# Performance work log

Measured on AMD Instinct MI355X. Metric: run time of the kernel, lower is better.

## Reference

```python
import jax, jax.numpy as jnp
import numpy as np

H, D, EPS = 4, 16, 1e-5
N_NODES, N_EDGES, F_IN, HID, N_GRAPHS, N_CLASSES = 100000, 1600000, 128, 64, 512, 10


def _bn(x, g, b, m, v):
    # BatchNorm1d in eval mode: running stats
    return (x - m) * jax.lax.rsqrt(v + EPS) * g + b


def _tconv(x, src, dst, wq, bq, wk, bk, wv, bv, ws, bs):
    # PyG TransformerConv: q from dst node, k/v from src node, scatter-softmax over dst,
    # scatter-add aggregation, concat heads, plus root (skip) linear. Dropout=eval (identity).
    N = x.shape[0]
    q = (x @ wq + bq).reshape(N, H, D)
    k = (x @ wk + bk).reshape(N, H, D)
    v = (x @ wv + bv).reshape(N, H, D)
    alpha = (q[dst] * k[src]).sum(-1) * np.float32(1.0 / np.sqrt(D))  # [E, H]
    amax = jax.ops.segment_max(alpha, dst, num_segments=N)            # [N, H]
    amax = jnp.where(jnp.isfinite(amax), amax, 0.0)
    ex = jnp.exp(alpha - amax[dst])
    denom = jax.ops.segment_sum(ex, dst, num_segments=N)
    attn = ex / (denom[dst] + 1e-16)                                  # [E, H]
    agg = jax.ops.segment_sum(attn[:, :, None] * v[src], dst, num_segments=N)  # [N, H, D]
    return agg.reshape(N, H * D) + x @ ws + bs


def setup_inputs() -> dict:
    key = jax.random.key(0)
    ks = list(jax.random.split(key, 40))
    def w(i, shape):
        return jax.random.normal(ks[i], shape, jnp.float32) * 0.05
    inp = {}
    inp['x'] = jax.random.normal(ks[0], (N_NODES, F_IN), jnp.float32)
    inp['edge_index'] = jax.random.randint(ks[1], (2, N_EDGES), 0, N_NODES, dtype=jnp.int32)
    inp['batch'] = jnp.sort(jax.random.randint(ks[2], (N_NODES,), 0, N_GRAPHS, dtype=jnp.int32))
    i = 3
    for p, fin in (('c1', F_IN), ('c2', HID)):
        for nm in ('wq', 'wk', 'wv', 'ws'):
            inp[p + '_' + nm] = w(i, (fin, HID)); i += 1
            inp[p + '_b' + nm[1]] = w(i, (HID,)); i += 1
    for p in ('bn1', 'bn2', 'clbn'):
        inp[p + '_g'] = jnp.ones((HID,), jnp.float32)
        inp[p + '_b'] = jnp.zeros((HID,), jnp.float32)
        inp[p + '_m'] = jnp.zeros((HID,), jnp.float32)
        inp[p + '_v'] = jnp.ones((HID,), jnp.float32)
    for nm, shp in (('p1_w', (HID, HID)), ('p2_w', (HID, HID)), ('cl1_w', (HID, HID)), ('cl2_w', (HID, N_CLASSES))):
        inp[nm] = w(i, shp); i += 1
    inp['p1_b'] = jnp.zeros((HID,), jnp.float32)
    inp['p2_b'] = jnp.zeros((HID,), jnp.float32)
    inp['cl1_b'] = jnp.zeros((HID,), jnp.float32)
    inp['cl2_b'] = jnp.zeros((N_CLASSES,), jnp.float32)
    return inp


def reference(x, edge_index, batch,
              c1_wq, c1_bq, c1_wk, c1_bk, c1_wv, c1_bv, c1_ws, c1_bs,
              bn1_g, bn1_b, bn1_m, bn1_v,
              c2_wq, c2_bq, c2_wk, c2_bk, c2_wv, c2_bv, c2_ws, c2_bs,
              bn2_g, bn2_b, bn2_m, bn2_v,
              p1_w, p1_b, p2_w, p2_b,
              cl1_w, cl1_b, clbn_g, clbn_b, clbn_m, clbn_v, cl2_w, cl2_b):
    src, dst = edge_index[0], edge_index[1]
    h = _tconv(x, src, dst, c1_wq, c1_bq, c1_wk, c1_bk, c1_wv, c1_bv, c1_ws, c1_bs)
    h = jax.nn.relu(_bn(h, bn1_g, bn1_b, bn1_m, bn1_v))
    h = _tconv(h, src, dst, c2_wq, c2_bq, c2_wk, c2_bk, c2_wv, c2_bv, c2_ws, c2_bs)
    h = jax.nn.relu(_bn(h, bn2_g, bn2_b, bn2_m, bn2_v))
    g = jax.ops.segment_max(h, batch, num_segments=N_GRAPHS)  # global_max_pool [G, HID]
    g = jnp.where(jnp.isfinite(g), g, 0.0)
    g = jax.nn.relu(g @ p1_w + p1_b) @ p2_w + p2_b
    g = jax.nn.relu(_bn(g @ cl1_w + cl1_b, clbn_g, clbn_b, clbn_m, clbn_v))
    logits = g @ cl2_w + cl2_b
    return jax.nn.log_softmax(logits, axis=1)
```

## Files before the change

### kernel.cpp

```cpp
#include <hip/hip_runtime.h>
#include <hip/hip_bf16.h>
#include <math.h>

constexpr int NN = 100000;
constexpr int EE = 1600000;
constexpr int GG = 512;
constexpr int MPAD = 100096;
constexpr int NBUCK = 782;
constexpr int EPB = 8192;
constexpr int CAP = 4096;

typedef __attribute__((ext_vector_type(8))) short short8;
typedef __attribute__((ext_vector_type(4))) float floatx4;

__device__ __forceinline__ unsigned short f2bf_rne(float f) {
    unsigned int u = __float_as_uint(f);
    u += 0x7fff + ((u >> 16) & 1);
    return (unsigned short)(u >> 16);
}
__device__ __forceinline__ float bf_lo(unsigned int u) { return __uint_as_float(u << 16); }
__device__ __forceinline__ float bf_hi(unsigned int u) { return __uint_as_float(u & 0xffff0000u); }

template<int C>
__device__ __forceinline__ float dppadd(float x) {
    int t = __builtin_amdgcn_update_dpp(0, __float_as_int(x), C, 0xf, 0xf, true);
    return x + __int_as_float(t);
}

__device__ __forceinline__ float dot8(uint4 kd, const float* q) {
    float p =      bf_lo(kd.x) * q[0];
    p = fmaf(bf_hi(kd.x), q[1], p);
    p = fmaf(bf_lo(kd.y), q[2], p);
    p = fmaf(bf_hi(kd.y), q[3], p);
    p = fmaf(bf_lo(kd.z), q[4], p);
    p = fmaf(bf_hi(kd.z), q[5], p);
    p = fmaf(bf_lo(kd.w), q[6], p);
    p = fmaf(bf_hi(kd.w), q[7], p);
    return p;
}
__device__ __forceinline__ void acc8(float* a, float e, uint4 vd) {
    a[0] = fmaf(e, bf_lo(vd.x), a[0]);
    a[1] = fmaf(e, bf_hi(vd.x), a[1]);
    a[2] = fmaf(e, bf_lo(vd.y), a[2]);
    a[3] = fmaf(e, bf_hi(vd.y), a[3]);
    a[4] = fmaf(e, bf_lo(vd.z), a[4]);
    a[5] = fmaf(e, bf_hi(vd.z), a[5]);
    a[6] = fmaf(e, bf_lo(vd.w), a[6]);
    a[7] = fmaf(e, bf_hi(vd.w), a[7]);
}

__global__ __launch_bounds__(512) void k_part(const int* __restrict__ src,
                                              const int* __restrict__ dst,
                                              int* __restrict__ bcur,
                                              unsigned int* __restrict__ ppair) {
    __shared__ int cnt[NBUCK];
    __shared__ int base[NBUCK];
    int tid = threadIdx.x;
    int e0 = blockIdx.x * EPB;
    for (int j = tid; j < NBUCK; j += 512) cnt[j] = 0;
    __syncthreads();
    int myd[16], myr[16];
    #pragma unroll
    for (int t = 0; t < 16; t++) {
        int i = e0 + t * 512 + tid;
        if (i < EE) {
            int d = dst[i];
            myd[t] = d;
            myr[t] = atomicAdd(&cnt[d >> 7], 1);
        } else myd[t] = -1;
    }
    __syncthreads();
    for (int j = tid; j < NBUCK; j += 512) base[j] = atomicAdd(&bcur[j], cnt[j]);
    __syncthreads();
    #pragma unroll
    for (int t = 0; t < 16; t++) {
        int i = e0 + t * 512 + tid;
        if (myd[t] >= 0) {
            int b = myd[t] >> 7;
            int pos = base[b] + myr[t];
            if (pos < CAP)
                ppair[(size_t)b * CAP + pos] =
                    ((unsigned int)src[i] << 7) | (unsigned int)(myd[t] & 127);
        }
    }
}

__global__ __launch_bounds__(256) void k_bucket(const unsigned int* __restrict__ ppair,
                                                const int* __restrict__ bcur,
                                                int* __restrict__ rowbeg,
                                                int* __restrict__ rowend,
                                                int* __restrict__ csr) {
    __shared__ int cnt[128];
    __shared__ int sa[128], sb[128];
    __shared__ int cur[128];
    int t = threadIdx.x;
    int b = blockIdx.x;
    int n = bcur[b]; if (n > CAP) n = CAP;
    int start = b * CAP;
    if (t < 128) cnt[t] = 0;
    __syncthreads();
    for (int i = t; i < n; i += 256)
        atomicAdd(&cnt[ppair[start + i] & 127], 1);
    __syncthreads();
    if (t < 128) sa[t] = cnt[t];
    __syncthreads();
    int* p = sa; int* q = sb;
    for (int off = 1; off < 128; off <<= 1) {
        if (t < 128) q[t] = (t >= off) ? (p[t] + p[t - off]) : p[t];
        __syncthreads();
        int* tmp = p; p = q; q = tmp;
    }
    if (t < 128) {
        int excl = (t == 0) ? 0 : p[t - 1];
        rowbeg[b * 128 + t] = start + excl;
        rowend[b * 128 + t] = start + p[t];
        cur[t] = start + excl;
    }
    __syncthreads();
    for (int i = t; i < n; i += 256) {
        unsigned int e = ppair[start + i];
        int pos = atomicAdd(&cur[e & 127], 1);
        csr[pos] = (int)(e >> 7);
    }
}

__global__ __launch_bounds__(256) void k_cvt_all(
    const float* __restrict__ w1q, const float* __restrict__ b1q,
    const float* __restrict__ w1k, const float* __restrict__ b1k,
    const float* __restrict__ w1v, const float* __restrict__ b1v,
    const float* __restrict__ w1s, const float* __restrict__ b1s,
    const float* __restrict__ w2q, const float* __restrict__ b2q,
    const float* __restrict__ w2k, const float* __restrict__ b2k,
    const float* __restrict__ w2v, const float* __restrict__ b2v,
    const float* __restrict__ w2s, const float* __restrict__ b2s,
    const float* __restrict__ bn1g, const float* __restrict__ bn1b,
    const float* __restrict__ bn1m, const float* __restrict__ bn1v,
    const float* __restrict__ bn2g, const float* __restrict__ bn2b,
    const float* __restrict__ bn2m, const float* __restrict__ bn2v,
    unsigned short* __restrict__ Bt1, float* __restrict__ bias1,
    unsigned short* __restrict__ Bt2, float* __restrict__ bias2,
    float* __restrict__ bnp, float* __restrict__ g0) {
    int b = blockIdx.x, tid = threadIdx.x;
    if (b == 0 && tid < 128) {
        int layer = tid >> 6, f = tid & 63;
        float gg = layer ? bn2g[f] : bn1g[f];
        float bb = layer ? bn2b[f] : bn1b[f];
        float mm = layer ? bn2m[f] : bn1m[f];
        float vv = layer ? bn2v[f] : bn1v[f];
        float sc = gg * rsqrtf(vv + 1e-5f);
        bnp[layer * 128 + f] = sc;
        bnp[layer * 128 + 64 + f] = bb - mm * sc;
    }
    if (b < 128) {
        g0[b * 256 + tid] = 0.f;
        int idx = b * 256 + tid;
        int col = idx >> 7, k = idx & 127;
        float val;
        if (col < 64)        val = w1k[k * 64 + col];
        else if (col < 128)  val = w1v[k * 64 + (col - 64)];
        else if (col < 192)  val = w1q[k * 64 + (col - 128)];
        else                 val = w1s[k * 64 + (col - 192)];
        Bt1[col * 128 + k] = f2bf_rne(val);
        if (k == 0) {
            float bv;
            if (col < 64)        bv = b1k[col];
            else if (col < 128)  bv = b1v[col - 64];
            else if (col < 192)  bv = b1q[col - 128];
            else                 bv = b1s[col - 192];
            bias1[col] = bv;
        }
    } else {
        int idx = (b - 128) * 256 + tid;
        int col = idx >> 6, k = idx & 63;
        float val;
        if (col < 64)        val = w2k[k * 64 + col];
        else if (col < 128)  val = w2v[k * 64 + (col - 64)];
        else if (col < 192)  val = w2q[k * 64 + (col - 128)];
        else                 val = w2s[k * 64 + (col - 192)];
        Bt2[col * 64 + k] = f2bf_rne(val);
        if (k == 0) {
            float bv;
            if (col < 64)        bv = b2k[col];
            else if (col < 128)  bv = b2v[col - 64];
            else if (col < 192)  bv = b2q[col - 128];
            else                 bv = b2s[col - 192];
            bias2[col] = bv;
        }
    }
}

template<int K, bool AF32>
__global__ __launch_bounds__(512) void gemm_mfma(
    const void* __restrict__ Araw,
    const unsigned short* __restrict__ Bt,
    const float* __restrict__ bias,
    unsigned short* __restrict__ out0,
    unsigned short* __restrict__ out1) {
    constexpr int SP = 72;
    __shared__ short As[128 * SP];
    __shared__ short Bs[256 * SP];
    int tid = threadIdx.x;
    int wave = tid >> 6, lane = tid & 63;
    int wm = wave >> 2, wn = wave & 3;
    int quad = lane >> 4, l16 = lane & 15;
    int rowBase = blockIdx.x * 128;

    floatx4 acc[4][4];
    #pragma unroll
    for (int i = 0; i < 4; i++)
        #pragma unroll
        for (int j = 0; j < 4; j++) acc[i][j] = (floatx4)0.f;

    for (int kc = 0; kc < K; kc += 64) {
        #pragma unroll
        for (int it = 0; it < 2; it++) {
            int flat = it * 512 + tid;
            int r = flat >> 3, c8 = (flat & 7) * 8;
            int ar = rowBase + r; if (ar >= NN) ar = NN - 1;
            short8 va;
            if constexpr (AF32) {
                const float* ap = (const float*)Araw + (size_t)ar * K + kc + c8;
                float4 u0 = *reinterpret_cast<const float4*>(ap);
                float4 u1 = *reinterpret_cast<const float4*>(ap + 4);
                va[0] = (short)f2bf_rne(u0.x); va[1] = (short)f2bf_rne(u0.y);
                va[2] = (short)f2bf_rne(u0.z); va[3] = (short)f2bf_rne(u0.w);
                va[4] = (short)f2bf_rne(u1.x); va[5] = (short)f2bf_rne(u1.y);
                va[6] = (short)f2bf_rne(u1.z); va[7] = (short)f2bf_rne(u1.w);
            } else {
                va = *reinterpret_cast<const short8*>(
                        (const unsigned short*)Araw + (size_t)ar * K + kc + c8);
            }
            *reinterpret_cast<short8*>(&As[r * SP + c8]) = va;
        }
        #pragma unroll
        for (int it = 0; it < 4; it++) {
            int flat = it * 512 + tid;
            int r = flat >> 3, c8 = (flat & 7) * 8;
            short8 vb = *reinterpret_cast<const short8*>(Bt + (size_t)r * K + kc + c8);
            *reinterpret_cast<short8*>(&Bs[r * SP + c8]) = vb;
        }
        __syncthreads();
        #pragma unroll
        for (int ks = 0; ks < 2; ks++) {
            short8 af[4], bf[4];
            #pragma unroll
            for (int i = 0; i < 4; i++)
                af[i] = *reinterpret_cast<const short8*>(&As[(wm * 64 + i * 16 + l16) * SP + ks * 32 + quad * 8]);
            #pragma unroll
            for (int j = 0; j < 4; j++)
                bf[j] = *reinterpret_cast<const short8*>(&Bs[(wn * 64 + j * 16 + l16) * SP + ks * 32 + quad * 8]);
            #pragma unroll
            for (int i = 0; i < 4; i++)
                #pragma unroll
                for (int j = 0; j < 4; j++)
                    acc[i][j] = __builtin_amdgcn_mfma_f32_16x16x32_bf16(af[i], bf[j], acc[i][j], 0, 0, 0);
        }
        __syncthreads();
    }

    unsigned short* outp = (wn < 2) ? out0 : out1;
    int colBase = (wn & 1) * 64;
    float bj[4];
    #pragma unroll
    for (int j = 0; j < 4; j++) bj[j] = bias[wn * 64 + j * 16 + l16];
    #pragma unroll
    for (int i = 0; i < 4; i++) {
        #pragma unroll
        for (int j = 0; j < 4; j++) {
            int col = colBase + j * 16 + l16;
            #pragma unroll
            for (int r = 0; r < 4; r++) {
                int row = rowBase + wm * 64 + i * 16 + quad * 4 + r;
                if (row < NN)
                    outp[(size_t)row * 128 + col] = f2bf_rne(acc[i][j][r] + bj[j]);
            }
        }
    }
}

__global__ __launch_bounds__(256) void attn_fused(
    const unsigned short* __restrict__ qsb,
    const unsigned char* __restrict__ kvb,
    const int* __restrict__ rowbeg,
    const int* __restrict__ rowend,
    const int* __restrict__ csr,
    const float* __restrict__ bnscale, const float* __restrict__ bnshift,
    uint4* __restrict__ h_out) {
    int wid = (blockIdx.x * 256 + threadIdx.x) >> 6;
    int lane = threadIdx.x & 63;
    if (wid >= NN) return;
    int g = lane >> 3, l8 = lane & 7;
    unsigned int qb16 = (unsigned int)(l8 << 4);
    const uint4* qrow = reinterpret_cast<const uint4*>(qsb + (size_t)wid * 128);
    const float SC = 0.3606737602222409f;
    uint4 qd = qrow[l8];
    float q[8];
    q[0] = bf_lo(qd.x) * SC; q[1] = bf_hi(qd.x) * SC;
    q[2] = bf_lo(qd.y) * SC; q[3] = bf_hi(qd.y) * SC;
    q[4] = bf_lo(qd.z) * SC; q[5] = bf_hi(qd.z) * SC;
    q[6] = bf_lo(qd.w) * SC; q[7] = bf_hi(qd.w) * SC;
    int jb = rowbeg[wid], je = rowend[wid];
    float a[8] = {0.f, 0.f, 0.f, 0.f, 0.f, 0.f, 0.f, 0.f};
    float denom = 0.f;
    int j = jb;
    for (; j + 15 < je; j += 16) {
        unsigned int oA = ((unsigned int)csr[j + g] << 8) + qb16;
        unsigned int oB = ((unsigned int)csr[j + 8 + g] << 8) + qb16;
        uint4 kA = *reinterpret_cast<const uint4*>(kvb + oA);
        uint4 vA = *reinterpret_cast<const uint4*>(kvb + oA + 128);
        uint4 kB = *reinterpret_cast<const uint4*>(kvb + oB);
        uint4 vB = *reinterpret_cast<const uint4*>(kvb + oB + 128);
        float pA = dppadd<0xB1>(dot8(kA, q));
        float pB = dppadd<0xB1>(dot8(kB, q));
        float eA = exp2f(pA), eB = exp2f(pB);
        denom += eA + eB;
        acc8(a, eA, vA);
        acc8(a, eB, vB);
    }
    for (; j < je; j += 8) {
        int jj = j + g;
        bool valid = jj < je;
        unsigned int o = ((unsigned int)csr[valid ? jj : je - 1] << 8) + qb16;
        uint4 kd = *reinterpret_cast<const uint4*>(kvb + o);
        uint4 vd = *reinterpret_cast<const uint4*>(kvb + o + 128);
        float p = dppadd<0xB1>(dot8(kd, q));
        float e = valid ? exp2f(p) : 0.f;
        denom += e;
        acc8(a, e, vd);
    }
    #pragma unroll
    for (int i = 0; i < 8; i++) {
        a[i] += __shfl_xor(a[i], 8);
        a[i] += __shfl_xor(a[i], 16);
        a[i] += __shfl_xor(a[i], 32);
    }
    denom += __shfl_xor(denom, 8);
    denom += __shfl_xor(denom, 16);
    denom += __shfl_xor(denom, 32);
    float inv = 1.f / (denom + 1e-16f);
    uint4 sd = qrow[8 + l8];
    float s[8];
    s[0] = bf_lo(sd.x); s[1] = bf_hi(sd.x);
    s[2] = bf_lo(sd.y); s[3] = bf_hi(sd.y);
    s[4] = bf_lo(sd.z); s[5] = bf_hi(sd.z);
    s[6] = bf_lo(sd.w); s[7] = bf_hi(sd.w);
    const float4* scp = reinterpret_cast<const float4*>(bnscale);
    const float4* shp = reinterpret_cast<const float4*>(bnshift);
    float4 sc0 = scp[l8 * 2], sc1 = scp[l8 * 2 + 1];
    float4 sh0 = shp[l8 * 2], sh1 = shp[l8 * 2 + 1];
    float o0 = fmaxf(fmaf(a[0] * inv + s[0], sc0.x, sh0.x), 0.f);
    float o1 = fmaxf(fmaf(a[1] * inv + s[1], sc0.y, sh0.y), 0.f);
    float o2 = fmaxf(fmaf(a[2] * inv + s[2], sc0.z, sh0.z), 0.f);
    float o3 = fmaxf(fmaf(a[3] * inv + s[3], sc0.w, sh0.w), 0.f);
    float o4 = fmaxf(fmaf(a[4] * inv + s[4], sc1.x, sh1.x), 0.f);
    float o5 = fmaxf(fmaf(a[5] * inv + s[5], sc1.y, sh1.y), 0.f);
    float o6 = fmaxf(fmaf(a[6] * inv + s[6], sc1.z, sh1.z), 0.f);
    float o7 = fmaxf(fmaf(a[7] * inv + s[7], sc1.w, sh1.w), 0.f);
    if (g == 0) {
        uint4 hw;
        hw.x = (unsigned int)f2bf_rne(o0) | ((unsigned int)f2bf_rne(o1) << 16);
        hw.y = (unsigned int)f2bf_rne(o2) | ((unsigned int)f2bf_rne(o3) << 16);
        hw.z = (unsigned int)f2bf_rne(o4) | ((unsigned int)f2bf_rne(o5) << 16);
        hw.w = (unsigned int)f2bf_rne(o6) | ((unsigned int)f2bf_rne(o7) << 16);
        h_out[(size_t)wid * 8 + l8] = hw;
    }
}

__global__ __launch_bounds__(256) void k_pool(const unsigned short* __restrict__ h,
                                              const int* __restrict__ batch,
                                              float* __restrict__ g0) {
    int f = threadIdx.x & 63;
    int sub = threadIdx.x >> 6;
    int n0 = blockIdx.x * 128;
    int nEnd = n0 + 128; if (nEnd > NN) nEnd = NN;
    int cur_g = -1; float cur_m = 0.f;
    for (int n = n0 + sub; n < nEnd; n += 4) {
        int bg = batch[n];
        float val = __uint_as_float((unsigned int)h[(size_t)n * 64 + f] << 16);
        if (bg != cur_g) {
            if (cur_g >= 0) atomicMax((int*)&g0[cur_g * 64 + f], __float_as_int(cur_m));
            cur_g = bg; cur_m = val;
        } else {
            cur_m = fmaxf(cur_m, val);
        }
    }
    if (cur_g >= 0) atomicMax((int*)&g0[cur_g * 64 + f], __float_as_int(cur_m));
}

__global__ __launch_bounds__(256) void k_mlp(
    const float* __restrict__ g0,
    const float* __restrict__ p1w, const float* __restrict__ p1b,
    const float* __restrict__ p2w, const float* __restrict__ p2b,
    const float* __restrict__ cl1w, const float* __restrict__ cl1b,
    const float* __restrict__ bg, const float* __restrict__ bb,
    const float* __restrict__ bm, const float* __restrict__ bv,
    const float* __restrict__ cl2w, const float* __restrict__ cl2b,
    float* __restrict__ outp) {
    __shared__ float w1[64 * 64], w2[64 * 64], w3[64 * 64], w4[64 * 10];
    __shared__ float sb1[64], sb2[64], sb3[64], sbn[4 * 64], sb4[10];
    int tid = threadIdx.x;
    for (int i = tid; i < 64 * 64; i += 256) { w1[i] = p1w[i]; w2[i] = p2w[i]; w3[i] = cl1w[i]; }
    for (int i = tid; i < 64 * 10; i += 256) w4[i] = cl2w[i];
    if (tid < 64) {
        sb1[tid] = p1b[tid]; sb2[tid] = p2b[tid]; sb3[tid] = cl1b[tid];
        sbn[tid] = bg[tid]; sbn[64 + tid] = bb[tid];
        sbn[128 + tid] = bm[tid]; sbn[192 + tid] = bv[tid];
    }
    if (tid < 10) sb4[tid] = cl2b[tid];
    __syncthreads();
    int lane = tid & 63, w = tid >> 6;
    int row = blockIdx.x * 4 + w;
    float x = g0[row * 64 + lane];
    if (!isfinite(x)) x = 0.f;
    float a = sb1[lane];
    for (int k = 0; k < 64; k++) a += __shfl(x, k) * w1[k * 64 + lane];
    x = fmaxf(a, 0.f);
    a = sb2[lane];
    for (int k = 0; k < 64; k++) a += __shfl(x, k) * w2[k * 64 + lane];
    x = a;
    a = sb3[lane];
    for (int k = 0; k < 64; k++) a += __shfl(x, k) * w3[k * 64 + lane];
    a = (a - sbn[128 + lane]) * rsqrtf(sbn[192 + lane] + 1e-5f) * sbn[lane] + sbn[64 + lane];
    x = fmaxf(a, 0.f);
    float lg[10];
    #pragma unroll
    for (int c = 0; c < 10; c++) {
        float p = x * w4[lane * 10 + c];
        p += __shfl_xor(p, 1);  p += __shfl_xor(p, 2);  p += __shfl_xor(p, 4);
        p += __shfl_xor(p, 8);  p += __shfl_xor(p, 16); p += __shfl_xor(p, 32);
        lg[c] = p + sb4[c];
    }
    float mx = lg[0];
    #pragma unroll
    for (int c = 1; c < 10; c++) mx = fmaxf(mx, lg[c]);
    float s = 0.f;
    #pragma unroll
    for (int c = 0; c < 10; c++) s += __expf(lg[c] - mx);
    float lse = mx + logf(s);
    float o = 0.f;
    #pragma unroll
    for (int c = 0; c < 10; c++) if (lane == c) o = lg[c];
    if (lane < 10) outp[row * 10 + lane] = o - lse;
}

extern "C" void kernel_launch(void* const* d_in, const int* in_sizes, int n_in,
                              void* d_out, int out_size, void* d_ws, size_t ws_size,
                              hipStream_t stream) {
    const float* x     = (const float*)d_in[0];
    const int*   ei    = (const int*)d_in[1];
    const int*   batch = (const int*)d_in[2];
    const float *c1_wq = (const float*)d_in[3],  *c1_bq = (const float*)d_in[4];
    const float *c1_wk = (const float*)d_in[5],  *c1_bk = (const float*)d_in[6];
    const float *c1_wv = (const float*)d_in[7],  *c1_bv = (const float*)d_in[8];
    const float *c1_ws = (const float*)d_in[9],  *c1_bs = (const float*)d_in[10];
    const float *c2_wq = (const float*)d_in[11], *c2_bq = (const float*)d_in[12];
    const float *c2_wk = (const float*)d_in[13], *c2_bk = (const float*)d_in[14];
    const float *c2_wv = (const float*)d_in[15], *c2_bv = (const float*)d_in[16];
    const float *c2_ws = (const float*)d_in[17], *c2_bs = (const float*)d_in[18];
    const float *bn1_g = (const float*)d_in[19], *bn1_b = (const float*)d_in[20];
    const float *bn1_m = (const float*)d_in[21], *bn1_v = (const float*)d_in[22];
    const float *bn2_g = (const float*)d_in[23], *bn2_b = (const float*)d_in[24];
    const float *bn2_m = (const float*)d_in[25], *bn2_v = (const float*)d_in[26];
    const float *clbn_g = (const float*)d_in[27], *clbn_b = (const float*)d_in[28];
    const float *clbn_m = (const float*)d_in[29], *clbn_v = (const float*)d_in[30];
    const float *p1_w = (const float*)d_in[31], *p2_w = (const float*)d_in[32];
    const float *cl1_w = (const float*)d_in[33], *cl2_w = (const float*)d_in[34];
    const float *p1_b = (const float*)d_in[35], *p2_b = (const float*)d_in[36];
    const float *cl1_b = (const float*)d_in[37], *cl2_b = (const float*)d_in[38];

    char* ws = (char*)d_ws;
    unsigned short* kv     = (unsigned short*)(ws);
    unsigned short* qsb    = (unsigned short*)(ws + 25600000);
    unsigned short* hbuf   = (unsigned short*)(ws + 51200000);
    unsigned int*   ppair  = (unsigned int*)(ws + 64012288);
    int*            csr    = (int*)(ws + 76824576);
    int*            rowbeg = (int*)(ws + 89636864);
    int*            rowend = (int*)(ws + 90037248);
    int*            bcur   = (int*)(ws + 90437632);
    float*          g0     = (float*)(ws + 90440768);
    unsigned short* Bt1    = (unsigned short*)(ws + 90571840);
    float*          b1     = (float*)(ws + 90637376);
    unsigned short* Bt2    = (unsigned short*)(ws + 90638400);
    float*          b2     = (float*)(ws + 90671168);
    float*          bnp    = (float*)(ws + 90672192);

    const int* srcIdx = ei;
    const int* dstIdx = ei + EE;

    hipMemsetAsync(bcur, 0, NBUCK * sizeof(int), stream);

    k_cvt_all<<<192, 256, 0, stream>>>(c1_wq, c1_bq, c1_wk, c1_bk, c1_wv, c1_bv,
                                       c1_ws, c1_bs,
                                       c2_wq, c2_bq, c2_wk, c2_bk, c2_wv, c2_bv,
                                       c2_ws, c2_bs,
                                       bn1_g, bn1_b, bn1_m, bn1_v,
                                       bn2_g, bn2_b, bn2_m, bn2_v,
                                       Bt1, b1, Bt2, b2, bnp, g0);

    constexpr int PBLK = (EE + EPB - 1) / EPB;
    k_part<<<PBLK, 512, 0, stream>>>(srcIdx, dstIdx, bcur, ppair);
    k_bucket<<<NBUCK, 256, 0, stream>>>(ppair, bcur, rowbeg, rowend, csr);

    gemm_mfma<128, true><<<MPAD / 128, 512, 0, stream>>>(x, Bt1, b1, kv, qsb);
    attn_fused<<<NN / 4, 256, 0, stream>>>(qsb, (const unsigned char*)kv,
                                           rowbeg, rowend, csr,
                                           bnp, bnp + 64, (uint4*)hbuf);

    gemm_mfma<64, false><<<MPAD / 128, 512, 0, stream>>>(hbuf, Bt2, b2, kv, qsb);
    attn_fused<<<NN / 4, 256, 0, stream>>>(qsb, (const unsigned char*)kv,
                                           rowbeg, rowend, csr,
                                           bnp + 128, bnp + 192, (uint4*)hbuf);

    k_pool<<<(NN + 127) / 128, 256, 0, stream>>>(hbuf, batch, g0);
    k_mlp<<<GG / 4, 256, 0, stream>>>(g0, p1_w, p1_b, p2_w, p2_b, cl1_w, cl1_b,
                                      clbn_g, clbn_b, clbn_m, clbn_v, cl2_w, cl2_b,
                                      (float*)d_out);
}
```

Before: 389.9 us.

## Co-schedule edge partitioning with first GEMM in one launch and widen pool loads

Merges the edge-bucketing partition kernel and the layer-1 projection GEMM into a single launch, with block index selecting the role, so the memory-bound partition work overlaps the MFMA GEMM. Also folds the bucket-counter memset into the weight-conversion kernel, halves edges per partition block, raises bucket kernel threads to 512, and has the pool kernel load two bf16 features per thread. This trades a larger shared-memory footprint for partition blocks (sized for the GEMM) against fewer launches and better overlap.

```diff
diff --git a/kernel.cpp b/kernel.cpp
--- a/kernel.cpp
+++ b/kernel.cpp
@@ -7,8 +7,10 @@
 constexpr int GG = 512;
 constexpr int MPAD = 100096;
 constexpr int NBUCK = 782;
-constexpr int EPB = 8192;
+constexpr int EPB = 4096;
 constexpr int CAP = 4096;
+constexpr int GB1 = MPAD / 128;
+constexpr int PBLK = (EE + EPB - 1) / EPB;
 
 typedef __attribute__((ext_vector_type(8))) short short8;
 typedef __attribute__((ext_vector_type(4))) float floatx4;
@@ -49,19 +51,20 @@
     a[7] = fmaf(e, bf_hi(vd.w), a[7]);
 }
 
-__global__ __launch_bounds__(512) void k_part(const int* __restrict__ src,
-                                              const int* __restrict__ dst,
-                                              int* __restrict__ bcur,
-                                              unsigned int* __restrict__ ppair) {
-    __shared__ int cnt[NBUCK];
-    __shared__ int base[NBUCK];
+__device__ void part_body(int bb, const int* __restrict__ src,
+                          const int* __restrict__ dst,
+                          int* __restrict__ bcur,
+                          unsigned int* __restrict__ ppair,
+                          char* smem) {
+    int* cnt  = reinterpret_cast<int*>(smem);
+    int* base = cnt + NBUCK;
     int tid = threadIdx.x;
-    int e0 = blockIdx.x * EPB;
+    int e0 = bb * EPB;
     for (int j = tid; j < NBUCK; j += 512) cnt[j] = 0;
     __syncthreads();
-    int myd[16], myr[16];
-    #pragma unroll
-    for (int t = 0; t < 16; t++) {
+    int myd[8], myr[8];
+    #pragma unroll
+    for (int t = 0; t < 8; t++) {
         int i = e0 + t * 512 + tid;
         if (i < EE) {
             int d = dst[i];
@@ -73,7 +76,7 @@
     for (int j = tid; j < NBUCK; j += 512) base[j] = atomicAdd(&bcur[j], cnt[j]);
     __syncthreads();
     #pragma unroll
-    for (int t = 0; t < 16; t++) {
+    for (int t = 0; t < 8; t++) {
         int i = e0 + t * 512 + tid;
         if (myd[t] >= 0) {
             int b = myd[t] >> 7;
@@ -85,125 +88,21 @@
     }
 }
 
-__global__ __launch_bounds__(256) void k_bucket(const unsigned int* __restrict__ ppair,
-                                                const int* __restrict__ bcur,
-                                                int* __restrict__ rowbeg,
-                                                int* __restrict__ rowend,
-                                                int* __restrict__ csr) {
-    __shared__ int cnt[128];
-    __shared__ int sa[128], sb[128];
-    __shared__ int cur[128];
-    int t = threadIdx.x;
-    int b = blockIdx.x;
-    int n = bcur[b]; if (n > CAP) n = CAP;
-    int start = b * CAP;
-    if (t < 128) cnt[t] = 0;
-    __syncthreads();
-    for (int i = t; i < n; i += 256)
-        atomicAdd(&cnt[ppair[start + i] & 127], 1);
-    __syncthreads();
-    if (t < 128) sa[t] = cnt[t];
-    __syncthreads();
-    int* p = sa; int* q = sb;
-    for (int off = 1; off < 128; off <<= 1) {
-        if (t < 128) q[t] = (t >= off) ? (p[t] + p[t - off]) : p[t];
-        __syncthreads();
-        int* tmp = p; p = q; q = tmp;
-    }
-    if (t < 128) {
-        int excl = (t == 0) ? 0 : p[t - 1];
-        rowbeg[b * 128 + t] = start + excl;
-        rowend[b * 128 + t] = start + p[t];
-        cur[t] = start + excl;
-    }
-    __syncthreads();
-    for (int i = t; i < n; i += 256) {
-        unsigned int e = ppair[start + i];
-        int pos = atomicAdd(&cur[e & 127], 1);
-        csr[pos] = (int)(e >> 7);
-    }
-}
-
-__global__ __launch_bounds__(256) void k_cvt_all(
-    const float* __restrict__ w1q, const float* __restrict__ b1q,
-    const float* __restrict__ w1k, const float* __restrict__ b1k,
-    const float* __restrict__ w1v, const float* __restrict__ b1v,
-    const float* __restrict__ w1s, const float* __restrict__ b1s,
-    const float* __restrict__ w2q, const float* __restrict__ b2q,
-    const float* __restrict__ w2k, const float* __restrict__ b2k,
-    const float* __restrict__ w2v, const float* __restrict__ b2v,
-    const float* __restrict__ w2s, const float* __restrict__ b2s,
-    const float* __restrict__ bn1g, const float* __restrict__ bn1b,
-    const float* __restrict__ bn1m, const float* __restrict__ bn1v,
-    const float* __restrict__ bn2g, const float* __restrict__ bn2b,
-    const float* __restrict__ bn2m, const float* __restrict__ bn2v,
-    unsigned short* __restrict__ Bt1, float* __restrict__ bias1,
-    unsigned short* __restrict__ Bt2, float* __restrict__ bias2,
-    float* __restrict__ bnp, float* __restrict__ g0) {
-    int b = blockIdx.x, tid = threadIdx.x;
-    if (b == 0 && tid < 128) {
-        int layer = tid >> 6, f = tid & 63;
-        float gg = layer ? bn2g[f] : bn1g[f];
-        float bb = layer ? bn2b[f] : bn1b[f];
-        float mm = layer ? bn2m[f] : bn1m[f];
-        float vv = layer ? bn2v[f] : bn1v[f];
-        float sc = gg * rsqrtf(vv + 1e-5f);
-        bnp[layer * 128 + f] = sc;
-        bnp[layer * 128 + 64 + f] = bb - mm * sc;
-    }
-    if (b < 128) {
-        g0[b * 256 + tid] = 0.f;
-        int idx = b * 256 + tid;
-        int col = idx >> 7, k = idx & 127;
-        float val;
-        if (col < 64)        val = w1k[k * 64 + col];
-        else if (col < 128)  val = w1v[k * 64 + (col - 64)];
-        else if (col < 192)  val = w1q[k * 64 + (col - 128)];
-        else                 val = w1s[k * 64 + (col - 192)];
-        Bt1[col * 128 + k] = f2bf_rne(val);
-        if (k == 0) {
-            float bv;
-            if (col < 64)        bv = b1k[col];
-            else if (col < 128)  bv = b1v[col - 64];
-            else if (col < 192)  bv = b1q[col - 128];
-            else                 bv = b1s[col - 192];
-            bias1[col] = bv;
-        }
-    } else {
-        int idx = (b - 128) * 256 + tid;
-        int col = idx >> 6, k = idx & 63;
-        float val;
-        if (col < 64)        val = w2k[k * 64 + col];
-        else if (col < 128)  val = w2v[k * 64 + (col - 64)];
-        else if (col < 192)  val = w2q[k * 64 + (col - 128)];
-        else                 val = w2s[k * 64 + (col - 192)];
-        Bt2[col * 64 + k] = f2bf_rne(val);
-        if (k == 0) {
-            float bv;
-            if (col < 64)        bv = b2k[col];
-            else if (col < 128)  bv = b2v[col - 64];
-            else if (col < 192)  bv = b2q[col - 128];
-            else                 bv = b2s[col - 192];
-            bias2[col] = bv;
-        }
-    }
-}
-
 template<int K, bool AF32>
-__global__ __launch_bounds__(512) void gemm_mfma(
-    const void* __restrict__ Araw,
-    const unsigned short* __restrict__ Bt,
-    const float* __restrict__ bias,
-    unsigned short* __restrict__ out0,
-    unsigned short* __restrict__ out1) {
+__device__ void gemm_body(int bb, const void* __restrict__ Araw,
+                          const unsigned short* __restrict__ Bt,
+                          const float* __restrict__ bias,
+                          unsigned short* __restrict__ out0,
+                          unsigned short* __restrict__ out1,
+                          char* smem) {
     constexpr int SP = 72;
-    __shared__ short As[128 * SP];
-    __shared__ short Bs[256 * SP];
+    short* As = reinterpret_cast<short*>(smem);
+    short* Bs = reinterpret_cast<short*>(smem + 18432);
     int tid = threadIdx.x;
     int wave = tid >> 6, lane = tid & 63;
     int wm = wave >> 2, wn = wave & 3;
     int quad = lane >> 4, l16 = lane & 15;
-    int rowBase = blockIdx.x * 128;
+    int rowBase = bb * 128;
 
     floatx4 acc[4][4];
     #pragma unroll
@@ -274,6 +173,142 @@
                 if (row < NN)
                     outp[(size_t)row * 128 + col] = f2bf_rne(acc[i][j][r] + bj[j]);
             }
+        }
+    }
+}
+
+__global__ __launch_bounds__(512) void k_gemm1_part(
+    const float* __restrict__ x,
+    const unsigned short* __restrict__ Bt,
+    const float* __restrict__ bias,
+    unsigned short* __restrict__ out0,
+    unsigned short* __restrict__ out1,
+    const int* __restrict__ src,
+    const int* __restrict__ dst,
+    int* __restrict__ bcur,
+    unsigned int* __restrict__ ppair) {
+    __shared__ __align__(16) char smem[55296];
+    if (blockIdx.x < PBLK)
+        part_body(blockIdx.x, src, dst, bcur, ppair, smem);
+    else
+        gemm_body<128, true>(blockIdx.x - PBLK, x, Bt, bias, out0, out1, smem);
+}
+
+__global__ __launch_bounds__(512) void k_gemm2(
+    const unsigned short* __restrict__ A,
+    const unsigned short* __restrict__ Bt,
+    const float* __restrict__ bias,
+    unsigned short* __restrict__ out0,
+    unsigned short* __restrict__ out1) {
+    __shared__ __align__(16) char smem[55296];
+    gemm_body<64, false>(blockIdx.x, A, Bt, bias, out0, out1, smem);
+}
+
+__global__ __launch_bounds__(512) void k_bucket(const unsigned int* __restrict__ ppair,
+                                                const int* __restrict__ bcur,
+                                                int* __restrict__ rowbeg,
+                                                int* __restrict__ rowend,
+                                                int* __restrict__ csr) {
+    __shared__ int cnt[128];
+    __shared__ int sa[128], sb[128];
+    __shared__ int cur[128];
+    int t = threadIdx.x;
+    int b = blockIdx.x;
+    int n = bcur[b]; if (n > CAP) n = CAP;
+    int start = b * CAP;
+    if (t < 128) cnt[t] = 0;
+    __syncthreads();
+    for (int i = t; i < n; i += 512)
+        atomicAdd(&cnt[ppair[start + i] & 127], 1);
+    __syncthreads();
+    if (t < 128) sa[t] = cnt[t];
+    __syncthreads();
+    int* p = sa; int* q = sb;
+    for (int off = 1; off < 128; off <<= 1) {
+        if (t < 128) q[t] = (t >= off) ? (p[t] + p[t - off]) : p[t];
+        __syncthreads();
+        int* tmp = p; p = q; q = tmp;
+    }
+    if (t < 128) {
+        int excl = (t == 0) ? 0 : p[t - 1];
+        rowbeg[b * 128 + t] = start + excl;
+        rowend[b * 128 + t] = start + p[t];
+        cur[t] = start + excl;
+    }
+    __syncthreads();
+    for (int i = t; i < n; i += 512) {
+        unsigned int e = ppair[start + i];
+        int pos = atomicAdd(&cur[e & 127], 1);
+        csr[pos] = (int)(e >> 7);
+    }
+}
+
+__global__ __launch_bounds__(256) void k_cvt_all(
+    const float* __restrict__ w1q, const float* __restrict__ b1q,
+    const float* __restrict__ w1k, const float* __restrict__ b1k,
+    const float* __restrict__ w1v, const float* __restrict__ b1v,
+    const float* __restrict__ w1s, const float* __restrict__ b1s,
+    const float* __restrict__ w2q, const float* __restrict__ b2q,
+    const float* __restrict__ w2k, const float* __restrict__ b2k,
+    const float* __restrict__ w2v, const float* __restrict__ b2v,
+    const float* __restrict__ w2s, const float* __restrict__ b2s,
+    const float* __restrict__ bn1g, const float* __restrict__ bn1b,
+    const float* __restrict__ bn1m, const float* __restrict__ bn1v,
+    const float* __restrict__ bn2g, const float* __restrict__ bn2b,
+    const float* __restrict__ bn2m, const float* __restrict__ bn2v,
+    unsigned short* __restrict__ Bt1, float* __restrict__ bias1,
+    unsigned short* __restrict__ Bt2, float* __restrict__ bias2,
+    float* __restrict__ bnp, float* __restrict__ g0,
+    int* __restrict__ bcur) {
+    int b = blockIdx.x, tid = threadIdx.x;
+    if (b < 4) {
+        int z = b * 256 + tid;
+        if (z < NBUCK) bcur[z] = 0;
+    }
+    if (b == 0 && tid < 128) {
+        int layer = tid >> 6, f = tid & 63;
+        float gg = layer ? bn2g[f] : bn1g[f];
+        float bb = layer ? bn2b[f] : bn1b[f];
+        float mm = layer ? bn2m[f] : bn1m[f];
+        float vv = layer ? bn2v[f] : bn1v[f];
+        float sc = gg * rsqrtf(vv + 1e-5f);
+        bnp[layer * 128 + f] = sc;
+        bnp[layer * 128 + 64 + f] = bb - mm * sc;
+    }
+    if (b < 128) {
+        g0[b * 256 + tid] = 0.f;
+        int idx = b * 256 + tid;
+        int col = idx >> 7, k = idx & 127;
+        float val;
+        if (col < 64)        val = w1k[k * 64 + col];
+        else if (col < 128)  val = w1v[k * 64 + (col - 64)];
+        else if (col < 192)  val = w1q[k * 64 + (col - 128)];
+        else                 val = w1s[k * 64 + (col - 192)];
+        Bt1[col * 128 + k] = f2bf_rne(val);
+        if (k == 0) {
+            float bv;
+            if (col < 64)        bv = b1k[col];
+            else if (col < 128)  bv = b1v[col - 64];
+            else if (col < 192)  bv = b1q[col - 128];
+            else                 bv = b1s[col - 192];
+            bias1[col] = bv;
+        }
+    } else {
+        int idx = (b - 128) * 256 + tid;
+        int col = idx >> 6, k = idx & 63;
+        float val;
+        if (col < 64)        val = w2k[k * 64 + col];
+        else if (col < 128)  val = w2v[k * 64 + (col - 64)];
+        else if (col < 192)  val = w2q[k * 64 + (col - 128)];
+        else                 val = w2s[k * 64 + (col - 192)];
+        Bt2[col * 64 + k] = f2bf_rne(val);
+        if (k == 0) {
+            float bv;
+            if (col < 64)        bv = b2k[col];
+            else if (col < 128)  bv = b2v[col - 64];
+            else if (col < 192)  bv = b2q[col - 128];
+            else                 bv = b2s[col - 192];
+            bias2[col] = bv;
         }
     }
 }
@@ -366,25 +401,32 @@
     }
 }
 
-__global__ __launch_bounds__(256) void k_pool(const unsigned short* __restrict__ h,
+__global__ __launch_bounds__(256) void k_pool(const unsigned int* __restrict__ h2,
                                               const int* __restrict__ batch,
                                               float* __restrict__ g0) {
-    int f = threadIdx.x & 63;
-    int sub = threadIdx.x >> 6;
-    int n0 = blockIdx.x * 128;
-    int nEnd = n0 + 128; if (nEnd > NN) nEnd = NN;
-    int cur_g = -1; float cur_m = 0.f;
-    for (int n = n0 + sub; n < nEnd; n += 4) {
+    int u = threadIdx.x & 31;
+    int sub = threadIdx.x >> 5;
+    int n0 = blockIdx.x * 256;
+    int nEnd = n0 + 256; if (nEnd > NN) nEnd = NN;
+    int cur_g = -1; float m0 = 0.f, m1 = 0.f;
+    for (int n = n0 + sub; n < nEnd; n += 8) {
         int bg = batch[n];
-        float val = __uint_as_float((unsigned int)h[(size_t)n * 64 + f] << 16);
+        unsigned int hv = h2[(size_t)n * 32 + u];
+        float v0 = bf_lo(hv), v1 = bf_hi(hv);
         if (bg != cur_g) {
-            if (cur_g >= 0) atomicMax((int*)&g0[cur_g * 64 + f], __float_as_int(cur_m));
-            cur_g = bg; cur_m = val;
+            if (cur_g >= 0) {
+                atomicMax((int*)&g0[cur_g * 64 + 2 * u], __float_as_int(m0));
+                atomicMax((int*)&g0[cur_g * 64 + 2 * u + 1], __float_as_int(m1));
+            }
+            cur_g = bg; m0 = v0; m1 = v1;
         } else {
-            cur_m = fmaxf(cur_m, val);
-        }
-    }
-    if (cur_g >= 0) atomicMax((int*)&g0[cur_g * 64 + f], __float_as_int(cur_m));
+            m0 = fmaxf(m0, v0); m1 = fmaxf(m1, v1);
+        }
+    }
+    if (cur_g >= 0) {
+        atomicMax((int*)&g0[cur_g * 64 + 2 * u], __float_as_int(m0));
+        atomicMax((int*)&g0[cur_g * 64 + 2 * u + 1], __float_as_int(m1));
+    }
 }
 
 __global__ __launch_bounds__(256) void k_mlp(
@@ -487,31 +529,29 @@
     const int* srcIdx = ei;
     const int* dstIdx = ei + EE;
 
-    hipMemsetAsync(bcur, 0, NBUCK * sizeof(int), stream);
-
     k_cvt_all<<<192, 256, 0, stream>>>(c1_wq, c1_bq, c1_wk, c1_bk, c1_wv, c1_bv,
                                        c1_ws, c1_bs,
                                        c2_wq, c2_bq, c2_wk, c2_bk, c2_wv, c2_bv,
                                        c2_ws, c2_bs,
                                        bn1_g, bn1_b, bn1_m, bn1_v,
                                        bn2_g, bn2_b, bn2_m, bn2_v,
-                                       Bt1, b1, Bt2, b2, bnp, g0);
-
-    constexpr int PBLK = (EE + EPB - 1) / EPB;
-    k_part<<<PBLK, 512, 0, stream>>>(srcIdx, dstIdx, bcur, ppair);
-    k_bucket<<<NBUCK, 256, 0, stream>>>(ppair, bcur, rowbeg, rowend, csr);
-
-    gemm_mfma<128, true><<<MPAD / 128, 512, 0, stream>>>(x, Bt1, b1, kv, qsb);
+                                       Bt1, b1, Bt2, b2, bnp, g0, bcur);
+
+    k_gemm1_part<<<PBLK + GB1, 512, 0, stream>>>(x, Bt1, b1, kv, qsb,
+                                                 srcIdx, dstIdx, bcur, ppair);
+
+    k_bucket<<<NBUCK, 512, 0, stream>>>(ppair, bcur, rowbeg, rowend, csr);
+
     attn_fused<<<NN / 4, 256, 0, stream>>>(qsb, (const unsigned char*)kv,
                                            rowbeg, rowend, csr,
                                            bnp, bnp + 64, (uint4*)hbuf);
 
-    gemm_mfma<64, false><<<MPAD / 128, 512, 0, stream>>>(hbuf, Bt2, b2, kv, qsb);
+    k_gemm2<<<GB1, 512, 0, stream>>>(hbuf, Bt2, b2, kv, qsb);
     attn_fused<<<NN / 4, 256, 0, stream>>>(qsb, (const unsigned char*)kv,
                                            rowbeg, rowend, csr,
                                            bnp + 128, bnp + 192, (uint4*)hbuf);
 
-    k_pool<<<(NN + 127) / 128, 256, 0, stream>>>(hbuf, batch, g0);
+    k_pool<<<(NN + 255) / 256, 256, 0, stream>>>((const unsigned int*)hbuf, batch, g0);
     k_mlp<<<GG / 4, 256, 0, stream>>>(g0, p1_w, p1_b, p2_w, p2_b, cl1_w, cl1_b,
                                       clbn_g, clbn_b, clbn_m, clbn_v, cl2_w, cl2_b,
                                       (float*)d_out);
```

Result: no change. 397.2 us (+1.9%).
